# Performance work log

Measured on AMD Instinct MI355X. Metric: run time of the kernel, lower is better.

Reference implementation:

```python
import jax, jax.numpy as jnp
import numpy as np

B, T, D, H = 2, 2048, 1024, 16  # batch, seq, n_embed, n_head


def setup_inputs() -> dict:
    key = jax.random.key(0)
    ks = jax.random.split(key, 5)
    scale = 1.0 / np.sqrt(D)
    return {
        "x": jax.random.normal(ks[0], (B, T, D), dtype=jnp.float32),
        "Wq": jax.random.normal(ks[1], (D, D), dtype=jnp.float32) * scale,
        "Wk": jax.random.normal(ks[2], (D, D), dtype=jnp.float32) * scale,
        "Wv": jax.random.normal(ks[3], (D, D), dtype=jnp.float32) * scale,
        "Wo": jax.random.normal(ks[4], (D, D), dtype=jnp.float32) * scale,
    }


def reference(x, Wq, Wk, Wv, Wo):
    b, t, d = x.shape
    hd = d // H  # head_dim
    # projections -> [B, H, T, hd]
    q = (x @ Wq).reshape(b, t, H, hd).transpose(0, 2, 1, 3)
    k = (x @ Wk).reshape(b, t, H, hd).transpose(0, 2, 1, 3)
    v = (x @ Wv).reshape(b, t, H, hd).transpose(0, 2, 1, 3)
    # scaled scores [B, H, T, T] with causal mask
    e = jnp.einsum("bhqd,bhkd->bhqk", q, k) * (1.0 / np.sqrt(hd))
    causal = jnp.tril(jnp.ones((t, t), dtype=bool))
    e = jnp.where(causal[None, None], e, jnp.finfo(e.dtype).min)
    alpha = jax.nn.softmax(e, axis=-1)
    # attention output -> [B, T, D]
    attn = jnp.einsum("bhqk,bhkd->bhqd", alpha, v)
    attn = attn.transpose(0, 2, 1, 3).reshape(b, t, d)
    return attn @ Wo
```

## Files before the change

kernel.cpp:

```cpp
#include <hip/hip_runtime.h>
#include <hip/hip_bf16.h>
#include <math.h>


#define Bsz  2
#define Tseq 2048
#define Dm   1024
#define NH   16
#define HD   64

typedef short bf16x8 __attribute__((ext_vector_type(8)));
typedef float floatx4 __attribute__((ext_vector_type(4)));

__device__ __forceinline__ unsigned short f2bf(float f) {
    __hip_bfloat16 h = __float2bfloat16(f);
    return *reinterpret_cast<unsigned short*>(&h);
}

__device__ __forceinline__ unsigned short f2bf_fast(float f) {
    unsigned int u = __builtin_bit_cast(unsigned int, f);
    return (unsigned short)((u + 0x8000u) >> 16);
}

__device__ __forceinline__ void lds16(unsigned short* lds, const unsigned short* g) {
    __builtin_amdgcn_global_load_lds(
        (const __attribute__((address_space(1))) void*)g,
        (__attribute__((address_space(3))) void*)lds, 16, 0, 0);
}

__global__ __launch_bounds__(256) void prep(const float* __restrict__ x,
                                            const float* __restrict__ W0,
                                            const float* __restrict__ W1,
                                            const float* __restrict__ W2,
                                            const float* __restrict__ W3,
                                            unsigned short* __restrict__ xb,
                                            unsigned short* __restrict__ T0,
                                            unsigned short* __restrict__ T1,
                                            unsigned short* __restrict__ T2,
                                            unsigned short* __restrict__ T3) {
    __shared__ float t[64][65];
    const int z = blockIdx.z;
    if (z >= 4) {
        const int bi = (z - 4) * 256 + blockIdx.y * 16 + blockIdx.x;
        const size_t i = (size_t)bi * 256 + threadIdx.x;
        const float4 v = ((const float4*)x)[i];
        ushort4 o;
        o.x = f2bf(v.x); o.y = f2bf(v.y); o.z = f2bf(v.z); o.w = f2bf(v.w);
        ((ushort4*)xb)[i] = o;
        return;
    }
    const float* W = (z == 0) ? W0 : (z == 1) ? W1 : (z == 2) ? W2 : W3;
    unsigned short* T = (z == 0) ? T0 : (z == 1) ? T1 : (z == 2) ? T2 : T3;
    const int k0 = blockIdx.y * 64, n0 = blockIdx.x * 64;
    const int row = threadIdx.x >> 6, col = threadIdx.x & 63;
#pragma unroll
    for (int p = 0; p < 16; ++p)
        t[p * 4 + row][col] = W[(size_t)(k0 + p * 4 + row) * Dm + n0 + col];
    __syncthreads();
#pragma unroll
    for (int p = 0; p < 16; ++p)
        T[(size_t)(n0 + p * 4 + row) * Dm + k0 + col] = f2bf(t[col][p * 4 + row]);
}

__device__ __forceinline__ void gemm128_mainloop(const unsigned short* __restrict__ A,
                                                 const unsigned short* __restrict__ Bt,
                                                 int K, int m0, int n0,
                                                 unsigned short* As, unsigned short* Bs,
                                                 floatx4 acc[4][4]) {
    const int tid = threadIdx.x;
    const int lane = tid & 63, wave = tid >> 6;
    const int l15 = lane & 15, quad = lane >> 4;
    const int wm = (wave >> 1) * 64, wn = (wave & 1) * 64;

    for (int k0 = 0; k0 < K; k0 += 32) {
        __syncthreads();
#pragma unroll
        for (int c = 0; c < 2; ++c) {
            const int idx = c * 256 + tid;
            const int row = idx >> 2, kc = (idx & 3) * 8;
            lds16(&As[row * 32 + kc], A + (size_t)(m0 + row) * K + k0 + kc);
            lds16(&Bs[row * 32 + kc], Bt + (size_t)(n0 + row) * K + k0 + kc);
        }
        __syncthreads();
        bf16x8 af[4], bf[4];
#pragma unroll
        for (int i = 0; i < 4; ++i)
            af[i] = *(const bf16x8*)&As[(wm + i * 16 + l15) * 32 + quad * 8];
#pragma unroll
        for (int j = 0; j < 4; ++j)
            bf[j] = *(const bf16x8*)&Bs[(wn + j * 16 + l15) * 32 + quad * 8];
#pragma unroll
        for (int i = 0; i < 4; ++i)
#pragma unroll
            for (int j = 0; j < 4; ++j)
                acc[i][j] = __builtin_amdgcn_mfma_f32_16x16x32_bf16(af[i], bf[j], acc[i][j], 0, 0, 0);
    }
}

__global__ __launch_bounds__(256) void gemm_qkv(const unsigned short* __restrict__ xb,
                                                const unsigned short* __restrict__ Wqt,
                                                const unsigned short* __restrict__ Wkt,
                                                const unsigned short* __restrict__ Wvt,
                                                unsigned short* __restrict__ Qb,
                                                unsigned short* __restrict__ Kb,
                                                unsigned short* __restrict__ VbT) {
    __shared__ unsigned short As[128 * 32];
    __shared__ unsigned short Bs[128 * 32];
    const int z = blockIdx.z;
    const unsigned short* Bt = (z == 0) ? Wqt : (z == 1) ? Wkt : Wvt;
    const float scale = (z == 0) ? (0.125f * 1.4426950408889634f) : 1.0f;
    const int m0 = blockIdx.y * 128, n0 = blockIdx.x * 128;

    floatx4 acc[4][4];
#pragma unroll
    for (int i = 0; i < 4; ++i)
#pragma unroll
        for (int j = 0; j < 4; ++j) acc[i][j] = (floatx4){0.f, 0.f, 0.f, 0.f};

    gemm128_mainloop(xb, Bt, Dm, m0, n0, As, Bs, acc);

    const int lane = threadIdx.x & 63, wave = threadIdx.x >> 6;
    const int l15 = lane & 15, quad = lane >> 4;
    const int wm = (wave >> 1) * 64, wn = (wave & 1) * 64;

    if (z == 2) {
#pragma unroll
        for (int i = 0; i < 4; ++i)
#pragma unroll
            for (int j = 0; j < 4; ++j) {
                const int col = n0 + wn + j * 16 + l15;
                const int hh = col >> 6, dd = col & 63;
                const int tok = m0 + wm + i * 16 + quad * 4;
                const int bb = tok >> 11, tl = tok & (Tseq - 1);
                ushort4 o;
                o.x = f2bf(acc[i][j][0]); o.y = f2bf(acc[i][j][1]);
                o.z = f2bf(acc[i][j][2]); o.w = f2bf(acc[i][j][3]);
                *(ushort4*)&VbT[((size_t)((bb * NH + hh) * HD + dd)) * Tseq + tl] = o;
            }
        return;
    }
    unsigned short* C = (z == 0) ? Qb : Kb;
#pragma unroll
    for (int i = 0; i < 4; ++i)
#pragma unroll
        for (int j = 0; j < 4; ++j)
#pragma unroll
            for (int r = 0; r < 4; ++r) {
                const int row = m0 + wm + i * 16 + quad * 4 + r;
                const int col = n0 + wn + j * 16 + l15;
                C[(size_t)row * Dm + col] = f2bf(acc[i][j][r] * scale);
            }
}

__global__ __launch_bounds__(256) void gemm_out(const unsigned short* __restrict__ Yb,
                                                const unsigned short* __restrict__ Wot,
                                                float* __restrict__ out) {
    __shared__ unsigned short As[64 * 32];
    __shared__ unsigned short Bs[64 * 32];
    const int m0 = blockIdx.y * 64, n0 = blockIdx.x * 64;
    const int tid = threadIdx.x;
    const int lane = tid & 63, wave = tid >> 6;
    const int l15 = lane & 15, quad = lane >> 4;
    const int wm = (wave >> 1) * 32, wn = (wave & 1) * 32;

    floatx4 acc[2][2];
#pragma unroll
    for (int i = 0; i < 2; ++i)
#pragma unroll
        for (int j = 0; j < 2; ++j) acc[i][j] = (floatx4){0.f, 0.f, 0.f, 0.f};

    const int srow = tid >> 2, kc = (tid & 3) * 8;

    for (int k0 = 0; k0 < Dm; k0 += 32) {
        __syncthreads();
        lds16(&As[srow * 32 + kc], Yb + (size_t)(m0 + srow) * Dm + k0 + kc);
        lds16(&Bs[srow * 32 + kc], Wot + (size_t)(n0 + srow) * Dm + k0 + kc);
        __syncthreads();
        bf16x8 af[2], bf[2];
#pragma unroll
        for (int i = 0; i < 2; ++i)
            af[i] = *(const bf16x8*)&As[(wm + i * 16 + l15) * 32 + quad * 8];
#pragma unroll
        for (int j = 0; j < 2; ++j)
            bf[j] = *(const bf16x8*)&Bs[(wn + j * 16 + l15) * 32 + quad * 8];
#pragma unroll
        for (int i = 0; i < 2; ++i)
#pragma unroll
            for (int j = 0; j < 2; ++j)
                acc[i][j] = __builtin_amdgcn_mfma_f32_16x16x32_bf16(af[i], bf[j], acc[i][j], 0, 0, 0);
    }

#pragma unroll
    for (int i = 0; i < 2; ++i)
#pragma unroll
        for (int j = 0; j < 2; ++j)
#pragma unroll
            for (int r = 0; r < 4; ++r) {
                const int row = m0 + wm + i * 16 + quad * 4 + r;
                const int col = n0 + wn + j * 16 + l15;
                out[(size_t)row * Dm + col] = acc[i][j][r];
            }
}

__global__ __launch_bounds__(256) void attn_mfma(const unsigned short* __restrict__ Qb,
                                                 const unsigned short* __restrict__ Kb,
                                                 const unsigned short* __restrict__ VbT,
                                                 unsigned short* __restrict__ Yb) {
    const int bh = blockIdx.x;
    const int b = bh >> 4;
    const int h = bh & 15;
    const int qt = 31 - blockIdx.y;
    const int tid = threadIdx.x;
    const int wave = tid >> 6;
    const int lane = tid & 63;
    const int l15 = lane & 15;
    const int quad = lane >> 4;

    __shared__ unsigned short Ks0[2][2][64][32];
    __shared__ unsigned short Ks1[2][2][64][32];
    __shared__ unsigned short Vt0[2][2][64][32];
    __shared__ unsigned short Vt1[2][2][64][32];
    __shared__ unsigned short Ps[4][16][72];

    const size_t tok0 = (size_t)b * Tseq;
    const int colh = h * HD;
    const unsigned short* vbase = VbT + (size_t)bh * HD * Tseq;

    const int qrow = qt * 64 + wave * 16;

    const unsigned short* qptr = Qb + (tok0 + qrow + l15) * Dm + colh + quad * 8;
    const bf16x8 qf0 = *(const bf16x8*)(qptr);
    const bf16x8 qf1 = *(const bf16x8*)(qptr + 32);

    float l_lane = 0.f;
    floatx4 o_acc[4];
#pragma unroll
    for (int t = 0; t < 4; ++t) o_acc[t] = (floatx4){0.f, 0.f, 0.f, 0.f};

    const int srow = tid >> 2;
    const int sc8 = (tid & 3) * 8;
    const int ssw = ((tid & 3) ^ ((srow >> 1) & 3)) * 8;
    const int qsw = (quad ^ ((l15 >> 1) & 3)) * 8;

    const int niter = (qt + 2) >> 1;

    {
        const unsigned short* krow0 = Kb + (tok0 + srow) * Dm + colh;
        const unsigned short* krow1 = Kb + (tok0 + 64 + srow) * Dm + colh;
        const unsigned short* vrow = vbase + (size_t)srow * Tseq;
        lds16(&Ks0[0][0][srow][sc8], krow0 + ssw);
        lds16(&Ks1[0][0][srow][sc8], krow0 + 32 + ssw);
        lds16(&Vt0[0][0][srow][sc8], vrow + ssw);
        lds16(&Vt1[0][0][srow][sc8], vrow + 32 + ssw);
        lds16(&Ks0[0][1][srow][sc8], krow1 + ssw);
        lds16(&Ks1[0][1][srow][sc8], krow1 + 32 + ssw);
        lds16(&Vt0[0][1][srow][sc8], vrow + 64 + ssw);
        lds16(&Vt1[0][1][srow][sc8], vrow + 64 + 32 + ssw);
    }
    asm volatile("s_waitcnt vmcnt(0)" ::: "memory");
    __builtin_amdgcn_s_barrier();
    __builtin_amdgcn_sched_barrier(0);

    for (int it = 0; it < niter; ++it) {
        const int k0 = it * 128;
        const int bi = it & 1;

        if (it + 1 < niter) {
            const int kn = k0 + 128;
#pragma unroll
            for (int s = 0; s < 2; ++s) {
                const unsigned short* krow = Kb + (tok0 + kn + s * 64 + srow) * Dm + colh;
                const unsigned short* vrow = vbase + (size_t)srow * Tseq + kn + s * 64;
                lds16(&Ks0[bi ^ 1][s][srow][sc8], krow + ssw);
                lds16(&Ks1[bi ^ 1][s][srow][sc8], krow + 32 + ssw);
                lds16(&Vt0[bi ^ 1][s][srow][sc8], vrow + ssw);
                lds16(&Vt1[bi ^ 1][s][srow][sc8], vrow + 32 + ssw);
            }
        }
        __builtin_amdgcn_sched_barrier(0);

#pragma unroll
        for (int s = 0; s < 2; ++s) {
            const int k0s = k0 + s * 64;
            if (k0s > qrow + 15) continue;

            floatx4 sf[4];
            __builtin_amdgcn_s_setprio(1);
#pragma unroll
            for (int t = 0; t < 4; ++t) {
                floatx4 c = (floatx4){0.f, 0.f, 0.f, 0.f};
                const bf16x8 kb0 = *(const bf16x8*)&Ks0[bi][s][t * 16 + l15][qsw];
                const bf16x8 kb1 = *(const bf16x8*)&Ks1[bi][s][t * 16 + l15][qsw];
                c = __builtin_amdgcn_mfma_f32_16x16x32_bf16(kb0, qf0, c, 0, 0, 0);
                c = __builtin_amdgcn_mfma_f32_16x16x32_bf16(kb1, qf1, c, 0, 0, 0);
                sf[t] = c;
            }
            __builtin_amdgcn_s_setprio(0);

            if (k0s + 63 > qrow) {
                const int ql = qrow + l15;
#pragma unroll
                for (int t = 0; t < 4; ++t)
#pragma unroll
                    for (int r = 0; r < 4; ++r) {
                        const int kl = k0s + t * 16 + quad * 4 + r;
                        if (kl > ql) sf[t][r] = -1.0e30f;
                    }
            }

#pragma unroll
            for (int t = 0; t < 4; ++t) {
                float p0 = __builtin_amdgcn_exp2f(sf[t][0]);
                float p1 = __builtin_amdgcn_exp2f(sf[t][1]);
                float p2 = __builtin_amdgcn_exp2f(sf[t][2]);
                float p3 = __builtin_amdgcn_exp2f(sf[t][3]);
                l_lane += (p0 + p1) + (p2 + p3);
                ushort4 o;
                o.x = f2bf_fast(p0); o.y = f2bf_fast(p1);
                o.z = f2bf_fast(p2); o.w = f2bf_fast(p3);
                *(ushort4*)&Ps[wave][l15][t * 16 + quad * 4] = o;
            }

            const bf16x8 pa0 = *(const bf16x8*)&Ps[wave][l15][quad * 8];
            const bf16x8 pa1 = *(const bf16x8*)&Ps[wave][l15][32 + quad * 8];
            __builtin_amdgcn_s_setprio(1);
#pragma unroll
            for (int t = 0; t < 4; ++t) {
                const bf16x8 vb0 = *(const bf16x8*)&Vt0[bi][s][t * 16 + l15][qsw];
                const bf16x8 vb1 = *(const bf16x8*)&Vt1[bi][s][t * 16 + l15][qsw];
                o_acc[t] = __builtin_amdgcn_mfma_f32_16x16x32_bf16(pa0, vb0, o_acc[t], 0, 0, 0);
                o_acc[t] = __builtin_amdgcn_mfma_f32_16x16x32_bf16(pa1, vb1, o_acc[t], 0, 0, 0);
            }
            __builtin_amdgcn_s_setprio(0);
        }

        asm volatile("s_waitcnt vmcnt(0)" ::: "memory");
        __builtin_amdgcn_s_barrier();
        __builtin_amdgcn_sched_barrier(0);
    }

    l_lane += __shfl_xor(l_lane, 16);
    l_lane += __shfl_xor(l_lane, 32);
    const float inv_q = 1.0f / l_lane;
    float inv_r[4];
#pragma unroll
    for (int r = 0; r < 4; ++r)
        inv_r[r] = __shfl(inv_q, (lane & 48) | (quad * 4 + r));
#pragma unroll
    for (int t = 0; t < 4; ++t)
#pragma unroll
        for (int r = 0; r < 4; ++r) {
            const int q = qrow + quad * 4 + r;
            Yb[(tok0 + q) * Dm + colh + t * 16 + l15] = f2bf(o_acc[t][r] * inv_r[r]);
        }
}

extern "C" void kernel_launch(void* const* d_in, const int* in_sizes, int n_in,
                              void* d_out, int out_size, void* d_ws, size_t ws_size,
                              hipStream_t stream) {
    const float* x  = (const float*)d_in[0];
    const float* Wq = (const float*)d_in[1];
    const float* Wk = (const float*)d_in[2];
    const float* Wv = (const float*)d_in[3];
    const float* Wo = (const float*)d_in[4];
    float* out = (float*)d_out;

    const int M = Bsz * Tseq;
    char* ws = (char*)d_ws;
    unsigned short* xb  = (unsigned short*)(ws);
    unsigned short* Wqt = (unsigned short*)(ws + (((size_t)8)  << 20));
    unsigned short* Wkt = (unsigned short*)(ws + (((size_t)10) << 20));
    unsigned short* Wvt = (unsigned short*)(ws + (((size_t)12) << 20));
    unsigned short* Wot = (unsigned short*)(ws + (((size_t)14) << 20));
    unsigned short* Qb  = (unsigned short*)(ws + (((size_t)16) << 20));
    unsigned short* Kb  = (unsigned short*)(ws + (((size_t)24) << 20));
    unsigned short* VbT = (unsigned short*)(ws + (((size_t)32) << 20));
    unsigned short* Yb  = (unsigned short*)(ws + (((size_t)40) << 20));

    dim3 blk(256);
    hipLaunchKernelGGL(prep, dim3(16, 16, 20), blk, 0, stream,
                       x, Wq, Wk, Wv, Wo, xb, Wqt, Wkt, Wvt, Wot);

    hipLaunchKernelGGL(gemm_qkv, dim3(Dm / 128, M / 128, 3), blk, 0, stream,
                       xb, Wqt, Wkt, Wvt, Qb, Kb, VbT);

    hipLaunchKernelGGL(attn_mfma, dim3(Bsz * NH, 32), blk, 0, stream, Qb, Kb, VbT, Yb);

    hipLaunchKernelGGL(gemm_out, dim3(Dm / 64, M / 64), blk, 0, stream, Yb, Wot, out);
}
```

Measured before the change: 173.2 us.

## Deepen GEMM K-tiles, enlarge output GEMM tile, use packed bf16 convert in attention

The QKV and output GEMMs now stage 64-wide K slices in LDS instead of 32, which halves the number of barrier pairs per K loop. The output GEMM tile grows from 64x64 to 128x64, so each wave computes 4x2 MFMA tiles and gets more reuse of each loaded A/B fragment. In the attention kernel, the software bf16 rounding of probabilities is replaced with the hardware v_cvt_pk_bf16_f32 packed conversion. In exchange, the larger tiles use more LDS and registers per block, and the output GEMM launches half as many blocks.

```diff
diff --git a/kernel.cpp b/kernel.cpp
--- a/kernel.cpp
+++ b/kernel.cpp
@@ -72,28 +72,31 @@
     const int l15 = lane & 15, quad = lane >> 4;
     const int wm = (wave >> 1) * 64, wn = (wave & 1) * 64;
 
-    for (int k0 = 0; k0 < K; k0 += 32) {
+    for (int k0 = 0; k0 < K; k0 += 64) {
         __syncthreads();
 #pragma unroll
-        for (int c = 0; c < 2; ++c) {
+        for (int c = 0; c < 4; ++c) {
             const int idx = c * 256 + tid;
-            const int row = idx >> 2, kc = (idx & 3) * 8;
-            lds16(&As[row * 32 + kc], A + (size_t)(m0 + row) * K + k0 + kc);
-            lds16(&Bs[row * 32 + kc], Bt + (size_t)(n0 + row) * K + k0 + kc);
+            const int row = idx >> 3, kc = (idx & 7) * 8;
+            lds16(&As[row * 64 + kc], A + (size_t)(m0 + row) * K + k0 + kc);
+            lds16(&Bs[row * 64 + kc], Bt + (size_t)(n0 + row) * K + k0 + kc);
         }
         __syncthreads();
-        bf16x8 af[4], bf[4];
-#pragma unroll
-        for (int i = 0; i < 4; ++i)
-            af[i] = *(const bf16x8*)&As[(wm + i * 16 + l15) * 32 + quad * 8];
-#pragma unroll
-        for (int j = 0; j < 4; ++j)
-            bf[j] = *(const bf16x8*)&Bs[(wn + j * 16 + l15) * 32 + quad * 8];
-#pragma unroll
-        for (int i = 0; i < 4; ++i)
+#pragma unroll
+        for (int kk = 0; kk < 2; ++kk) {
+            bf16x8 af[4], bfr[4];
+#pragma unroll
+            for (int i = 0; i < 4; ++i)
+                af[i] = *(const bf16x8*)&As[(wm + i * 16 + l15) * 64 + kk * 32 + quad * 8];
 #pragma unroll
             for (int j = 0; j < 4; ++j)
-                acc[i][j] = __builtin_amdgcn_mfma_f32_16x16x32_bf16(af[i], bf[j], acc[i][j], 0, 0, 0);
+                bfr[j] = *(const bf16x8*)&Bs[(wn + j * 16 + l15) * 64 + kk * 32 + quad * 8];
+#pragma unroll
+            for (int i = 0; i < 4; ++i)
+#pragma unroll
+                for (int j = 0; j < 4; ++j)
+                    acc[i][j] = __builtin_amdgcn_mfma_f32_16x16x32_bf16(af[i], bfr[j], acc[i][j], 0, 0, 0);
+        }
     }
 }
 
@@ -104,8 +107,8 @@
                                                 unsigned short* __restrict__ Qb,
                                                 unsigned short* __restrict__ Kb,
                                                 unsigned short* __restrict__ VbT) {
-    __shared__ unsigned short As[128 * 32];
-    __shared__ unsigned short Bs[128 * 32];
+    __shared__ unsigned short As[128 * 64];
+    __shared__ unsigned short Bs[128 * 64];
     const int z = blockIdx.z;
     const unsigned short* Bt = (z == 0) ? Wqt : (z == 1) ? Wkt : Wvt;
     const float scale = (z == 0) ? (0.125f * 1.4426950408889634f) : 1.0f;
@@ -155,43 +158,54 @@
 __global__ __launch_bounds__(256) void gemm_out(const unsigned short* __restrict__ Yb,
                                                 const unsigned short* __restrict__ Wot,
                                                 float* __restrict__ out) {
-    __shared__ unsigned short As[64 * 32];
-    __shared__ unsigned short Bs[64 * 32];
-    const int m0 = blockIdx.y * 64, n0 = blockIdx.x * 64;
+    __shared__ unsigned short As[128 * 64];
+    __shared__ unsigned short Bs[64 * 64];
+    const int m0 = blockIdx.y * 128, n0 = blockIdx.x * 64;
     const int tid = threadIdx.x;
     const int lane = tid & 63, wave = tid >> 6;
     const int l15 = lane & 15, quad = lane >> 4;
-    const int wm = (wave >> 1) * 32, wn = (wave & 1) * 32;
-
-    floatx4 acc[2][2];
-#pragma unroll
-    for (int i = 0; i < 2; ++i)
+    const int wm = (wave >> 1) * 64, wn = (wave & 1) * 32;
+
+    floatx4 acc[4][2];
+#pragma unroll
+    for (int i = 0; i < 4; ++i)
 #pragma unroll
         for (int j = 0; j < 2; ++j) acc[i][j] = (floatx4){0.f, 0.f, 0.f, 0.f};
 
-    const int srow = tid >> 2, kc = (tid & 3) * 8;
-
-    for (int k0 = 0; k0 < Dm; k0 += 32) {
+    for (int k0 = 0; k0 < Dm; k0 += 64) {
         __syncthreads();
-        lds16(&As[srow * 32 + kc], Yb + (size_t)(m0 + srow) * Dm + k0 + kc);
-        lds16(&Bs[srow * 32 + kc], Wot + (size_t)(n0 + srow) * Dm + k0 + kc);
+#pragma unroll
+        for (int c = 0; c < 4; ++c) {
+            const int idx = c * 256 + tid;
+            const int row = idx >> 3, kc = (idx & 7) * 8;
+            lds16(&As[row * 64 + kc], Yb + (size_t)(m0 + row) * Dm + k0 + kc);
+        }
+#pragma unroll
+        for (int c = 0; c < 2; ++c) {
+            const int idx = c * 256 + tid;
+            const int row = idx >> 3, kc = (idx & 7) * 8;
+            lds16(&Bs[row * 64 + kc], Wot + (size_t)(n0 + row) * Dm + k0 + kc);
+        }
         __syncthreads();
-        bf16x8 af[2], bf[2];
-#pragma unroll
-        for (int i = 0; i < 2; ++i)
-            af[i] = *(const bf16x8*)&As[(wm + i * 16 + l15) * 32 + quad * 8];
-#pragma unroll
-        for (int j = 0; j < 2; ++j)
-            bf[j] = *(const bf16x8*)&Bs[(wn + j * 16 + l15) * 32 + quad * 8];
-#pragma unroll
-        for (int i = 0; i < 2; ++i)
+#pragma unroll
+        for (int kk = 0; kk < 2; ++kk) {
+            bf16x8 af[4], bfr[2];
+#pragma unroll
+            for (int i = 0; i < 4; ++i)
+                af[i] = *(const bf16x8*)&As[(wm + i * 16 + l15) * 64 + kk * 32 + quad * 8];
 #pragma unroll
             for (int j = 0; j < 2; ++j)
-                acc[i][j] = __builtin_amdgcn_mfma_f32_16x16x32_bf16(af[i], bf[j], acc[i][j], 0, 0, 0);
-    }
-
-#pragma unroll
-    for (int i = 0; i < 2; ++i)
+                bfr[j] = *(const bf16x8*)&Bs[(wn + j * 16 + l15) * 64 + kk * 32 + quad * 8];
+#pragma unroll
+            for (int i = 0; i < 4; ++i)
+#pragma unroll
+                for (int j = 0; j < 2; ++j)
+                    acc[i][j] = __builtin_amdgcn_mfma_f32_16x16x32_bf16(af[i], bfr[j], acc[i][j], 0, 0, 0);
+        }
+    }
+
+#pragma unroll
+    for (int i = 0; i < 4; ++i)
 #pragma unroll
         for (int j = 0; j < 2; ++j)
 #pragma unroll
@@ -315,10 +329,11 @@
                 float p2 = __builtin_amdgcn_exp2f(sf[t][2]);
                 float p3 = __builtin_amdgcn_exp2f(sf[t][3]);
                 l_lane += (p0 + p1) + (p2 + p3);
-                ushort4 o;
-                o.x = f2bf_fast(p0); o.y = f2bf_fast(p1);
-                o.z = f2bf_fast(p2); o.w = f2bf_fast(p3);
-                *(ushort4*)&Ps[wave][l15][t * 16 + quad * 4] = o;
+                unsigned int w0, w1;
+                asm("v_cvt_pk_bf16_f32 %0, %1, %2" : "=v"(w0) : "v"(p0), "v"(p1));
+                asm("v_cvt_pk_bf16_f32 %0, %1, %2" : "=v"(w1) : "v"(p2), "v"(p3));
+                uint2 o; o.x = w0; o.y = w1;
+                *(uint2*)&Ps[wave][l15][t * 16 + quad * 4] = o;
             }
 
             const bf16x8 pa0 = *(const bf16x8*)&Ps[wave][l15][quad * 8];
@@ -386,5 +401,5 @@
 
     hipLaunchKernelGGL(attn_mfma, dim3(Bsz * NH, 32), blk, 0, stream, Qb, Kb, VbT, Yb);
 
-    hipLaunchKernelGGL(gemm_out, dim3(Dm / 64, M / 64), blk, 0, stream, Yb, Wot, out);
-}
+    hipLaunchKernelGGL(gemm_out, dim3(Dm / 64, M / 128), blk, 0, stream, Yb, Wot, out);
+}
```

Result: slower. 194.7 us (+12.4%).
